# Kernel optimization log

Hardware: AMD Instinct MI355X
Metric: run time of the kernel (lower is better)

The kernel has to match this reference:

```python
import jax, jax.numpy as jnp
import numpy as np

N_HEAD = 4
HIDDEN = 1024
D_HEAD = HIDDEN // N_HEAD  # 256
SEQ = 1024
BATCH = 16
NEG_INF = -1e9


def setup_inputs() -> dict:
    key = jax.random.key(0)
    k1, k2, k3 = jax.random.split(key, 3)
    x = jax.random.normal(k1, (BATCH, SEQ, HIDDEN), dtype=jnp.float32)
    # torch Linear(hidden, (2n+1)*d_head, bias=False); stored here as [in, out]
    w_qkv = jax.random.normal(k2, (HIDDEN, (2 * N_HEAD + 1) * D_HEAD), dtype=jnp.float32) * (HIDDEN ** -0.5)
    # out_proj: Linear(d_head, hidden, bias=False), stored as [d_head, hidden]
    w_out = jax.random.normal(k3, (D_HEAD, HIDDEN), dtype=jnp.float32) * (D_HEAD ** -0.5)
    return {"x": x, "w_qkv": w_qkv, "w_out": w_out}


def reference(x, w_qkv, w_out):
    bs, t, h = x.shape
    n_head, d_head = N_HEAD, D_HEAD
    scale = d_head ** -0.5
    qkv = x @ w_qkv  # [bs, t, (2n+1)*d]
    q = qkv[..., : n_head * d_head].reshape(bs, t, n_head, d_head)
    k = qkv[..., n_head * d_head : 2 * n_head * d_head].reshape(bs, t, n_head, d_head)
    v = qkv[..., 2 * n_head * d_head :]  # [bs, t, d] -- single shared V
    # scores [bs, n_head, t, s]
    scores = jnp.einsum("btnd,bsnd->bnts", q, k) * scale
    causal = jnp.triu(jnp.ones((t, t), dtype=bool), 1)  # True above diag
    scores = jnp.where(causal, NEG_INF, scores)
    attn_prob = jax.nn.softmax(scores, axis=-1)  # [bs, n_head, t, s]
    attn_vec = jnp.einsum("bnts,bsd->bntd", attn_prob, v)
    m_attn_vec = jnp.mean(attn_vec, axis=1)  # mean over heads -> [bs, t, d]
    out = m_attn_vec @ w_out  # [bs, t, hidden]
    return out, attn_prob
```

## Files before the change

kernel.cpp:

```cpp
#include <hip/hip_runtime.h>
#include <hip/hip_bf16.h>
#include <type_traits>

#define BATCH  16
#define SEQ    1024
#define HIDDEN 1024
#define NHEAD  4
#define DHEAD  256
#define QKVN   2304

typedef _Float16 f16x8 __attribute__((ext_vector_type(8)));
typedef float    f32x4 __attribute__((ext_vector_type(4)));

__device__ __forceinline__ void gll16(const void* g, void* l) {
  __builtin_amdgcn_global_load_lds(
      (const __attribute__((address_space(1))) unsigned int*)g,
      (__attribute__((address_space(3))) unsigned int*)l, 16, 0, 0);
}

__global__ __launch_bounds__(256) void f32_to_f16(
    const float* __restrict__ in, _Float16* __restrict__ out) {
  int i4 = blockIdx.x * 256 + threadIdx.x;
  float4 v = ((const float4*)in)[i4];
  _Float16 h4[4] = {(_Float16)v.x, (_Float16)v.y, (_Float16)v.z, (_Float16)v.w};
  *(uint2*)&out[(size_t)i4 * 4] = *(uint2*)h4;
}

__global__ __launch_bounds__(256) void transpose_to_f16(
    const float* __restrict__ in, _Float16* __restrict__ out, int R, int C) {
  __shared__ float tile[64][65];
  int bc = blockIdx.x * 64, br = blockIdx.y * 64;
  int t = threadIdx.x;
  int tr = t >> 6, tc = t & 63;
  for (int i = 0; i < 64; i += 4)
    tile[tr + i][tc] = in[(size_t)(br + tr + i) * C + bc + tc];
  __syncthreads();
  for (int i = 0; i < 64; i += 4)
    out[(size_t)(bc + tr + i) * R + br + tc] = (_Float16)tile[tc][tr + i];
}

__global__ __launch_bounds__(256) void transpose_v(
    const _Float16* __restrict__ qkv, _Float16* __restrict__ vT) {
  __shared__ _Float16 tile[64][65];
  int b = blockIdx.z;
  int s0 = blockIdx.x * 64, d0 = blockIdx.y * 64;
  int t = threadIdx.x;
  int tr = t >> 6, tc = t & 63;
  for (int i = 0; i < 64; i += 4)
    tile[tr + i][tc] = qkv[((size_t)(b * SEQ + s0 + tr + i)) * QKVN + 2 * NHEAD * DHEAD + d0 + tc];
  __syncthreads();
  for (int i = 0; i < 64; i += 4)
    vT[((size_t)(b * DHEAD + d0 + tr + i)) * SEQ + s0 + tc] = tile[tc][tr + i];
}

template <typename OT>
__global__ __launch_bounds__(256) void gemm_bt(
    const _Float16* __restrict__ A, const _Float16* __restrict__ B,
    OT* __restrict__ C, int M, int N, int K) {
  __shared__ __align__(16) _Float16 As[128][32];
  __shared__ __align__(16) _Float16 Bs[128][32];
  int bm = blockIdx.x * 128, bn = blockIdx.y * 128;
  int t = threadIdx.x;
  int w = t >> 6, L = t & 63, lane15 = L & 15, quad = L >> 4;
  int wr = (w >> 1) * 64, wc = (w & 1) * 64;
  f32x4 acc[4][4] = {};
  for (int k0 = 0; k0 < K; k0 += 32) {
    __syncthreads();
    for (int r = 0; r < 2; r++) {
      int u = t + r * 256;
      int row = u >> 2, c8 = u & 3;
      gll16(&A[(size_t)(bm + row) * K + k0 + c8 * 8], &As[row][c8 * 8]);
      gll16(&B[(size_t)(bn + row) * K + k0 + c8 * 8], &Bs[row][c8 * 8]);
    }
    __syncthreads();
    f16x8 af[4], bf[4];
    for (int i = 0; i < 4; i++) af[i] = *(f16x8*)&As[wr + i * 16 + lane15][quad * 8];
    for (int j = 0; j < 4; j++) bf[j] = *(f16x8*)&Bs[wc + j * 16 + lane15][quad * 8];
    for (int i = 0; i < 4; i++)
      for (int j = 0; j < 4; j++)
        acc[i][j] = __builtin_amdgcn_mfma_f32_16x16x32_f16(af[i], bf[j], acc[i][j], 0, 0, 0);
  }
  for (int i = 0; i < 4; i++)
    for (int j = 0; j < 4; j++) {
      int gr = bm + wr + i * 16 + quad * 4;
      int gc = bn + wc + j * 16 + lane15;
      for (int r = 0; r < 4; r++) {
        float v = acc[i][j][r];
        if constexpr (std::is_same_v<OT, float>)
          C[(size_t)(gr + r) * N + gc] = v;
        else
          C[(size_t)(gr + r) * N + gc] = (_Float16)v;
      }
    }
}

__global__ __launch_bounds__(512, 2) void scores_norm_kernel(
    const _Float16* __restrict__ qkv, float* __restrict__ P) {
  int ti = blockIdx.x, n = blockIdx.y, b = blockIdx.z;
  __shared__ __align__(16) _Float16 Qs[8][64][32];
  __shared__ __align__(16) _Float16 Ks[8][64][32];
  int t = threadIdx.x;
  int w = t >> 6, L = t & 63, lane15 = L & 15, quad = L >> 4;
  int r16 = (w & 3) * 16;
  int ch  = (w >> 2) * 32;
  for (int r = 0; r < 4; r++) {
    int u = t + r * 512;
    int kc = u >> 8, row = (u & 255) >> 2, c8 = u & 3;
    gll16(&qkv[((size_t)(b * SEQ + ti * 64 + row)) * QKVN + n * DHEAD + kc * 32 + c8 * 8],
          &Qs[kc][row][c8 * 8]);
  }
  float m[4], l[4];
  for (int r = 0; r < 4; r++) { m[r] = -INFINITY; l[r] = 0.f; }
  f32x4 s[16][2];
  int trow = ti * 64 + r16 + quad * 4;
  const float scale = 0.0625f;
#pragma unroll
  for (int si = 0; si < 16; si++) {
    if (si <= ti) {
      __syncthreads();
      for (int r = 0; r < 4; r++) {
        int u = t + r * 512;
        int kc = u >> 8, row = (u & 255) >> 2, c8 = u & 3;
        gll16(&qkv[((size_t)(b * SEQ + si * 64 + row)) * QKVN + NHEAD * DHEAD + n * DHEAD + kc * 32 + c8 * 8],
              &Ks[kc][row][c8 * 8]);
      }
      __syncthreads();
      s[si][0] = (f32x4){0.f, 0.f, 0.f, 0.f};
      s[si][1] = (f32x4){0.f, 0.f, 0.f, 0.f};
      for (int kc = 0; kc < 8; kc++) {
        f16x8 aq = *(f16x8*)&Qs[kc][r16 + lane15][quad * 8];
        for (int j = 0; j < 2; j++) {
          f16x8 bk = *(f16x8*)&Ks[kc][ch + j * 16 + lane15][quad * 8];
          s[si][j] = __builtin_amdgcn_mfma_f32_16x16x32_f16(aq, bk, s[si][j], 0, 0, 0);
        }
      }
      for (int j = 0; j < 2; j++) {
        int col = si * 64 + ch + j * 16 + lane15;
        for (int r = 0; r < 4; r++) {
          float v = s[si][j][r] * scale;
          if (col > trow + r) v = -1e9f;
          s[si][j][r] = v;
        }
      }
      for (int r = 0; r < 4; r++) {
        float mt = fmaxf(s[si][0][r], s[si][1][r]);
        for (int off = 1; off < 16; off <<= 1) mt = fmaxf(mt, __shfl_xor(mt, off, 64));
        float mn = fmaxf(m[r], mt);
        float sum = __expf(s[si][0][r] - mn) + __expf(s[si][1][r] - mn);
        for (int off = 1; off < 16; off <<= 1) sum += __shfl_xor(sum, off, 64);
        l[r] = l[r] * __expf(m[r] - mn) + sum;
        m[r] = mn;
      }
    }
  }
  __syncthreads();
  float* sM  = (float*)&Qs[0][0][0];
  float* sL  = sM + 128;
  float* sMc = sM + 256;
  float* sRl = sM + 320;
  if (lane15 == 0) {
    for (int r = 0; r < 4; r++) {
      sM[(w >> 2) * 64 + r16 + quad * 4 + r] = m[r];
      sL[(w >> 2) * 64 + r16 + quad * 4 + r] = l[r];
    }
  }
  __syncthreads();
  if (t < 64) {
    float m0 = sM[t], m1 = sM[64 + t], l0 = sL[t], l1 = sL[64 + t];
    float mc = fmaxf(m0, m1);
    float lc = l0 * __expf(m0 - mc) + l1 * __expf(m1 - mc);
    sMc[t] = mc;
    sRl[t] = 1.0f / lc;
  }
  __syncthreads();
  float mr[4], rl[4];
  for (int r = 0; r < 4; r++) {
    mr[r] = sMc[r16 + quad * 4 + r];
    rl[r] = sRl[r16 + quad * 4 + r];
  }
  size_t Pbase = ((size_t)(b * NHEAD + n)) * SEQ * SEQ;
#pragma unroll
  for (int si = 0; si < 16; si++) {
    if (si <= ti) {
      for (int j = 0; j < 2; j++) {
        int col = si * 64 + ch + j * 16 + lane15;
        for (int r = 0; r < 4; r++) {
          float p = (col > trow + r) ? 0.f : __expf(s[si][j][r] - mr[r]) * rl[r];
          P[Pbase + (size_t)(trow + r) * SEQ + col] = p;
        }
      }
    }
  }
  {
    float4 z = make_float4(0.f, 0.f, 0.f, 0.f);
    int c4min = (ti + 1) * 16;
    for (int u = t; u < 16384; u += 512) {
      int row = u >> 8, c4 = u & 255;
      if (c4 >= c4min)
        *(float4*)&P[Pbase + (size_t)(ti * 64 + row) * SEQ + c4 * 4] = z;
    }
  }
}

__global__ __launch_bounds__(256) void pmean_kernel(
    const float* __restrict__ P, _Float16* __restrict__ Pmean) {
  int si = blockIdx.x, ti = blockIdx.y, b = blockIdx.z;
  if (si > ti) return;
  int t = threadIdx.x;
  int row = t >> 2, c16 = (t & 3) * 16;
  size_t tile_off = (size_t)(ti * 64 + row) * SEQ + si * 64 + c16;
  float acc[16];
  for (int i = 0; i < 16; i++) acc[i] = 0.f;
  for (int n = 0; n < 4; n++) {
    const float* p = &P[((size_t)(b * NHEAD + n)) * SEQ * SEQ + tile_off];
    for (int q = 0; q < 4; q++) {
      float4 v = *(const float4*)(p + q * 4);
      acc[q * 4 + 0] += v.x; acc[q * 4 + 1] += v.y;
      acc[q * 4 + 2] += v.z; acc[q * 4 + 3] += v.w;
    }
  }
  _Float16 h[16];
  for (int i = 0; i < 16; i++) h[i] = (_Float16)(acc[i] * 0.25f);
  _Float16* pm = &Pmean[((size_t)(b * SEQ + ti * 64 + row)) * SEQ + si * 64 + c16];
  *(uint4*)pm = *(uint4*)h;
  *(uint4*)(pm + 8) = *(uint4*)(h + 8);
}

__global__ __launch_bounds__(256) void pv_kernel(
    const _Float16* __restrict__ Pmean, const _Float16* __restrict__ vT,
    _Float16* __restrict__ mattn) {
  int ti = blockIdx.x, b = blockIdx.y;
  __shared__ __align__(16) _Float16 Pm[2][64][32];
  __shared__ __align__(16) _Float16 Vs[2][256][32];
  int t = threadIdx.x;
  int w = t >> 6, L = t & 63, lane15 = L & 15, quad = L >> 4;
  f32x4 acc[16] = {};
  for (int si = 0; si <= ti; si++) {
    __syncthreads();
    for (int r = 0; r < 2; r++) {
      int u = t + r * 256;
      int kc = u >> 8, row = (u & 255) >> 2, c8 = u & 3;
      gll16(&Pmean[((size_t)(b * SEQ + ti * 64 + row)) * SEQ + si * 64 + kc * 32 + c8 * 8],
            &Pm[kc][row][c8 * 8]);
    }
    for (int r = 0; r < 8; r++) {
      int u = t + r * 256;
      int kc = u >> 10, d = (u & 1023) >> 2, c8 = u & 3;
      gll16(&vT[((size_t)(b * DHEAD + d)) * SEQ + si * 64 + kc * 32 + c8 * 8],
            &Vs[kc][d][c8 * 8]);
    }
    __syncthreads();
    for (int kc = 0; kc < 2; kc++) {
      f16x8 ap = *(f16x8*)&Pm[kc][w * 16 + lane15][quad * 8];
      for (int j = 0; j < 16; j++) {
        f16x8 bv = *(f16x8*)&Vs[kc][j * 16 + lane15][quad * 8];
        acc[j] = __builtin_amdgcn_mfma_f32_16x16x32_f16(ap, bv, acc[j], 0, 0, 0);
      }
    }
  }
  for (int j = 0; j < 16; j++) {
    int row = b * SEQ + ti * 64 + w * 16 + quad * 4;
    int col = j * 16 + lane15;
    for (int r = 0; r < 4; r++)
      mattn[(size_t)(row + r) * DHEAD + col] = (_Float16)acc[j][r];
  }
}

extern "C" void kernel_launch(void* const* d_in, const int* in_sizes, int n_in,
                              void* d_out, int out_size, void* d_ws, size_t ws_size,
                              hipStream_t stream) {
  const float* x     = (const float*)d_in[0];
  const float* w_qkv = (const float*)d_in[1];
  const float* w_out = (const float*)d_in[2];
  float* out = (float*)d_out;
  float* P   = out + (size_t)BATCH * SEQ * HIDDEN;

  _Float16* wqkvT = (_Float16*)d_ws;
  _Float16* woutT = wqkvT + (size_t)QKVN * HIDDEN;
  _Float16* qkvb  = woutT + (size_t)HIDDEN * DHEAD;
  _Float16* vT    = qkvb + (size_t)BATCH * SEQ * QKVN;
  _Float16* mattn = qkvb;
  _Float16* Pmean = qkvb + (size_t)BATCH * SEQ * DHEAD;
  _Float16* xh    = (_Float16*)P;

  f32_to_f16<<<BATCH * SEQ * HIDDEN / 1024, 256, 0, stream>>>(x, xh);
  transpose_to_f16<<<dim3(QKVN / 64, HIDDEN / 64), 256, 0, stream>>>(w_qkv, wqkvT, HIDDEN, QKVN);
  transpose_to_f16<<<dim3(HIDDEN / 64, DHEAD / 64), 256, 0, stream>>>(w_out, woutT, DHEAD, HIDDEN);
  gemm_bt<_Float16><<<dim3(BATCH * SEQ / 128, QKVN / 128), 256, 0, stream>>>(
      xh, wqkvT, qkvb, BATCH * SEQ, QKVN, HIDDEN);
  transpose_v<<<dim3(SEQ / 64, DHEAD / 64, BATCH), 256, 0, stream>>>(qkvb, vT);
  scores_norm_kernel<<<dim3(SEQ / 64, NHEAD, BATCH), 512, 0, stream>>>(qkvb, P);
  pmean_kernel<<<dim3(SEQ / 64, SEQ / 64, BATCH), 256, 0, stream>>>(P, Pmean);
  pv_kernel<<<dim3(SEQ / 64, BATCH), 256, 0, stream>>>(Pmean, vT, mattn);
  gemm_bt<float><<<dim3(BATCH * SEQ / 128, HIDDEN / 128), 256, 0, stream>>>(
      mattn, woutT, out, BATCH * SEQ, HIDDEN, DHEAD);
}
```

Measured before the change: 728.9 us.

## Double-buffer K and PV tiles, swizzle blocks, split PV by head-dim quarters

The scores kernel now double-buffers K tiles in LDS, holds the Q fragments in registers, and swaps the online softmax for a two-pass max-then-sum over the scores kept in registers. The final write becomes a single multiply by a per-row factor. The PV kernel splits the head dimension into four blocks for more parallelism, double-buffers its Pmean/V tiles, and both kernels swizzle block order across XCDs. This targets load latency, repeated shuffle reductions and poor occupancy, at the cost of more LDS and higher register pressure.

```diff
diff --git a/kernel.cpp b/kernel.cpp
--- a/kernel.cpp
+++ b/kernel.cpp
@@ -96,9 +96,11 @@
 
 __global__ __launch_bounds__(512, 2) void scores_norm_kernel(
     const _Float16* __restrict__ qkv, float* __restrict__ P) {
-  int ti = blockIdx.x, n = blockIdx.y, b = blockIdx.z;
+  int lin = blockIdx.x + 16 * (blockIdx.y + 4 * blockIdx.z);
+  int swz = (lin & 7) * 128 + (lin >> 3);
+  int ti = swz & 15, n = (swz >> 4) & 3, b = swz >> 6;
   __shared__ __align__(16) _Float16 Qs[8][64][32];
-  __shared__ __align__(16) _Float16 Ks[8][64][32];
+  __shared__ __align__(16) _Float16 Ks[2][8][64][32];
   int t = threadIdx.x;
   int w = t >> 6, L = t & 63, lane15 = L & 15, quad = L >> 4;
   int r16 = (w & 3) * 16;
@@ -108,50 +110,68 @@
     int kc = u >> 8, row = (u & 255) >> 2, c8 = u & 3;
     gll16(&qkv[((size_t)(b * SEQ + ti * 64 + row)) * QKVN + n * DHEAD + kc * 32 + c8 * 8],
           &Qs[kc][row][c8 * 8]);
-  }
-  float m[4], l[4];
-  for (int r = 0; r < 4; r++) { m[r] = -INFINITY; l[r] = 0.f; }
+    gll16(&qkv[((size_t)(b * SEQ + row)) * QKVN + NHEAD * DHEAD + n * DHEAD + kc * 32 + c8 * 8],
+          &Ks[0][kc][row][c8 * 8]);
+  }
+  __syncthreads();
+  f16x8 aq[8];
+#pragma unroll
+  for (int kc = 0; kc < 8; kc++) aq[kc] = *(f16x8*)&Qs[kc][r16 + lane15][quad * 8];
   f32x4 s[16][2];
   int trow = ti * 64 + r16 + quad * 4;
   const float scale = 0.0625f;
 #pragma unroll
   for (int si = 0; si < 16; si++) {
     if (si <= ti) {
-      __syncthreads();
-      for (int r = 0; r < 4; r++) {
-        int u = t + r * 512;
-        int kc = u >> 8, row = (u & 255) >> 2, c8 = u & 3;
-        gll16(&qkv[((size_t)(b * SEQ + si * 64 + row)) * QKVN + NHEAD * DHEAD + n * DHEAD + kc * 32 + c8 * 8],
-              &Ks[kc][row][c8 * 8]);
-      }
-      __syncthreads();
+      if (si < ti) {
+        for (int r = 0; r < 4; r++) {
+          int u = t + r * 512;
+          int kc = u >> 8, row = (u & 255) >> 2, c8 = u & 3;
+          gll16(&qkv[((size_t)(b * SEQ + (si + 1) * 64 + row)) * QKVN + NHEAD * DHEAD + n * DHEAD + kc * 32 + c8 * 8],
+                &Ks[(si + 1) & 1][kc][row][c8 * 8]);
+        }
+      }
       s[si][0] = (f32x4){0.f, 0.f, 0.f, 0.f};
       s[si][1] = (f32x4){0.f, 0.f, 0.f, 0.f};
       for (int kc = 0; kc < 8; kc++) {
-        f16x8 aq = *(f16x8*)&Qs[kc][r16 + lane15][quad * 8];
         for (int j = 0; j < 2; j++) {
-          f16x8 bk = *(f16x8*)&Ks[kc][ch + j * 16 + lane15][quad * 8];
-          s[si][j] = __builtin_amdgcn_mfma_f32_16x16x32_f16(aq, bk, s[si][j], 0, 0, 0);
+          f16x8 bk = *(f16x8*)&Ks[si & 1][kc][ch + j * 16 + lane15][quad * 8];
+          s[si][j] = __builtin_amdgcn_mfma_f32_16x16x32_f16(aq[kc], bk, s[si][j], 0, 0, 0);
         }
       }
-      for (int j = 0; j < 2; j++) {
-        int col = si * 64 + ch + j * 16 + lane15;
-        for (int r = 0; r < 4; r++) {
+      __syncthreads();
+    }
+  }
+  float m[4], l[4];
+#pragma unroll
+  for (int r = 0; r < 4; r++) {
+    float mx = -INFINITY;
+#pragma unroll
+    for (int si = 0; si < 16; si++) {
+      if (si <= ti) {
+        for (int j = 0; j < 2; j++) {
+          int col = si * 64 + ch + j * 16 + lane15;
           float v = s[si][j][r] * scale;
           if (col > trow + r) v = -1e9f;
           s[si][j][r] = v;
+          mx = fmaxf(mx, v);
         }
       }
-      for (int r = 0; r < 4; r++) {
-        float mt = fmaxf(s[si][0][r], s[si][1][r]);
-        for (int off = 1; off < 16; off <<= 1) mt = fmaxf(mt, __shfl_xor(mt, off, 64));
-        float mn = fmaxf(m[r], mt);
-        float sum = __expf(s[si][0][r] - mn) + __expf(s[si][1][r] - mn);
-        for (int off = 1; off < 16; off <<= 1) sum += __shfl_xor(sum, off, 64);
-        l[r] = l[r] * __expf(m[r] - mn) + sum;
-        m[r] = mn;
-      }
-    }
+    }
+    for (int off = 1; off < 16; off <<= 1) mx = fmaxf(mx, __shfl_xor(mx, off, 64));
+    float sum = 0.f;
+#pragma unroll
+    for (int si = 0; si < 16; si++) {
+      if (si <= ti) {
+        for (int j = 0; j < 2; j++) {
+          float p = __expf(s[si][j][r] - mx);
+          s[si][j][r] = p;
+          sum += p;
+        }
+      }
+    }
+    for (int off = 1; off < 16; off <<= 1) sum += __shfl_xor(sum, off, 64);
+    m[r] = mx; l[r] = sum;
   }
   __syncthreads();
   float* sM  = (float*)&Qs[0][0][0];
@@ -173,10 +193,10 @@
     sRl[t] = 1.0f / lc;
   }
   __syncthreads();
-  float mr[4], rl[4];
+  float fac[4];
   for (int r = 0; r < 4; r++) {
-    mr[r] = sMc[r16 + quad * 4 + r];
-    rl[r] = sRl[r16 + quad * 4 + r];
+    int row = r16 + quad * 4 + r;
+    fac[r] = __expf(m[r] - sMc[row]) * sRl[row];
   }
   size_t Pbase = ((size_t)(b * NHEAD + n)) * SEQ * SEQ;
 #pragma unroll
@@ -184,10 +204,8 @@
     if (si <= ti) {
       for (int j = 0; j < 2; j++) {
         int col = si * 64 + ch + j * 16 + lane15;
-        for (int r = 0; r < 4; r++) {
-          float p = (col > trow + r) ? 0.f : __expf(s[si][j][r] - mr[r]) * rl[r];
-          P[Pbase + (size_t)(trow + r) * SEQ + col] = p;
-        }
+        for (int r = 0; r < 4; r++)
+          P[Pbase + (size_t)(trow + r) * SEQ + col] = s[si][j][r] * fac[r];
       }
     }
   }
@@ -229,38 +247,49 @@
 __global__ __launch_bounds__(256) void pv_kernel(
     const _Float16* __restrict__ Pmean, const _Float16* __restrict__ vT,
     _Float16* __restrict__ mattn) {
-  int ti = blockIdx.x, b = blockIdx.y;
-  __shared__ __align__(16) _Float16 Pm[2][64][32];
-  __shared__ __align__(16) _Float16 Vs[2][256][32];
+  int lin = blockIdx.x + 16 * (blockIdx.y + 4 * blockIdx.z);
+  int swz = (lin & 7) * 128 + (lin >> 3);
+  int ti = swz & 15, dq = (swz >> 4) & 3, b = swz >> 6;
+  __shared__ __align__(16) _Float16 Pm[2][2][64][32];
+  __shared__ __align__(16) _Float16 Vs[2][2][64][32];
   int t = threadIdx.x;
   int w = t >> 6, L = t & 63, lane15 = L & 15, quad = L >> 4;
-  f32x4 acc[16] = {};
+  f32x4 acc[4] = {};
+  for (int r = 0; r < 2; r++) {
+    int u = t + r * 256;
+    int kc = u >> 8, row = (u & 255) >> 2, c8 = u & 3;
+    gll16(&Pmean[((size_t)(b * SEQ + ti * 64 + row)) * SEQ + kc * 32 + c8 * 8],
+          &Pm[0][kc][row][c8 * 8]);
+    gll16(&vT[((size_t)(b * DHEAD + dq * 64 + row)) * SEQ + kc * 32 + c8 * 8],
+          &Vs[0][kc][row][c8 * 8]);
+  }
+  __syncthreads();
   for (int si = 0; si <= ti; si++) {
+    int cb = si & 1;
+    if (si < ti) {
+      for (int r = 0; r < 2; r++) {
+        int u = t + r * 256;
+        int kc = u >> 8, row = (u & 255) >> 2, c8 = u & 3;
+        gll16(&Pmean[((size_t)(b * SEQ + ti * 64 + row)) * SEQ + (si + 1) * 64 + kc * 32 + c8 * 8],
+              &Pm[cb ^ 1][kc][row][c8 * 8]);
+        gll16(&vT[((size_t)(b * DHEAD + dq * 64 + row)) * SEQ + (si + 1) * 64 + kc * 32 + c8 * 8],
+              &Vs[cb ^ 1][kc][row][c8 * 8]);
+      }
+    }
+#pragma unroll
+    for (int kc = 0; kc < 2; kc++) {
+      f16x8 ap = *(f16x8*)&Pm[cb][kc][w * 16 + lane15][quad * 8];
+#pragma unroll
+      for (int j = 0; j < 4; j++) {
+        f16x8 bv = *(f16x8*)&Vs[cb][kc][j * 16 + lane15][quad * 8];
+        acc[j] = __builtin_amdgcn_mfma_f32_16x16x32_f16(ap, bv, acc[j], 0, 0, 0);
+      }
+    }
     __syncthreads();
-    for (int r = 0; r < 2; r++) {
-      int u = t + r * 256;
-      int kc = u >> 8, row = (u & 255) >> 2, c8 = u & 3;
-      gll16(&Pmean[((size_t)(b * SEQ + ti * 64 + row)) * SEQ + si * 64 + kc * 32 + c8 * 8],
-            &Pm[kc][row][c8 * 8]);
-    }
-    for (int r = 0; r < 8; r++) {
-      int u = t + r * 256;
-      int kc = u >> 10, d = (u & 1023) >> 2, c8 = u & 3;
-      gll16(&vT[((size_t)(b * DHEAD + d)) * SEQ + si * 64 + kc * 32 + c8 * 8],
-            &Vs[kc][d][c8 * 8]);
-    }
-    __syncthreads();
-    for (int kc = 0; kc < 2; kc++) {
-      f16x8 ap = *(f16x8*)&Pm[kc][w * 16 + lane15][quad * 8];
-      for (int j = 0; j < 16; j++) {
-        f16x8 bv = *(f16x8*)&Vs[kc][j * 16 + lane15][quad * 8];
-        acc[j] = __builtin_amdgcn_mfma_f32_16x16x32_f16(ap, bv, acc[j], 0, 0, 0);
-      }
-    }
-  }
-  for (int j = 0; j < 16; j++) {
+  }
+  for (int j = 0; j < 4; j++) {
     int row = b * SEQ + ti * 64 + w * 16 + quad * 4;
-    int col = j * 16 + lane15;
+    int col = dq * 64 + j * 16 + lane15;
     for (int r = 0; r < 4; r++)
       mattn[(size_t)(row + r) * DHEAD + col] = (_Float16)acc[j][r];
   }
@@ -291,7 +320,7 @@
   transpose_v<<<dim3(SEQ / 64, DHEAD / 64, BATCH), 256, 0, stream>>>(qkvb, vT);
   scores_norm_kernel<<<dim3(SEQ / 64, NHEAD, BATCH), 512, 0, stream>>>(qkvb, P);
   pmean_kernel<<<dim3(SEQ / 64, SEQ / 64, BATCH), 256, 0, stream>>>(P, Pmean);
-  pv_kernel<<<dim3(SEQ / 64, BATCH), 256, 0, stream>>>(Pmean, vT, mattn);
+  pv_kernel<<<dim3(SEQ / 64, 4, BATCH), 256, 0, stream>>>(Pmean, vT, mattn);
   gemm_bt<float><<<dim3(BATCH * SEQ / 128, HIDDEN / 128), 256, 0, stream>>>(
       mattn, woutT, out, BATCH * SEQ, HIDDEN, DHEAD);
 }
```

After: 638.9 us. -12.4%, faster.
